# Kernel tuning notes

Measured on AMD Instinct MI355X. Metric: run time of the kernel, lower is better.

The kernel has to match this reference:

```python
import jax, jax.numpy as jnp
import numpy as np

N = 100000
E = 1600000
F_IN = 128
F_OUT = 128


def setup_inputs() -> dict:
    key = jax.random.key(0)
    k1, k2, k3, k4 = jax.random.split(key, 4)
    x = jax.random.normal(k1, (N, F_IN), dtype=jnp.float32)
    edge_index = jax.random.randint(k2, (2, E), 0, N, dtype=jnp.int64)
    # GCNConv params (glorot weight, zero bias as in PyG defaults)
    limit = float(np.sqrt(6.0 / (F_IN + F_OUT)))
    W = jax.random.uniform(k3, (F_IN, F_OUT), minval=-limit, maxval=limit, dtype=jnp.float32)
    b = jnp.zeros((F_OUT,), dtype=jnp.float32)
    return {"x": x, "edge_index": edge_index, "W": W, "b": b}


def reference(x, edge_index, W, b):
    n = x.shape[0]
    # add self-loops
    loops = jnp.arange(n, dtype=edge_index.dtype)
    src = jnp.concatenate([edge_index[0], loops])  # source nodes j
    dst = jnp.concatenate([edge_index[1], loops])  # target nodes i
    # symmetric normalization: deg over incoming edges (targets), weight 1
    deg = jax.ops.segment_sum(jnp.ones_like(dst, dtype=x.dtype), dst, num_segments=n)
    dinv = jnp.where(deg > 0, jax.lax.rsqrt(deg), 0.0)
    norm = dinv[src] * dinv[dst]  # [E+N]
    # linear transform then message passing
    h = x @ W  # [N, F_OUT]
    msgs = h[src] * norm[:, None]  # gather + scale, [E+N, F_OUT]
    out = jax.ops.segment_sum(msgs, dst, num_segments=n)  # scatter-add
    return out + b
```

## Files before the change

### kernel.cpp

```cpp
#include <hip/hip_runtime.h>

#define FDIM 128
#define NBMAX 512
#define EPB 4096

typedef __attribute__((ext_vector_type(8))) short bf16x8;
typedef __attribute__((ext_vector_type(4))) float f32x4;

__device__ __forceinline__ unsigned short f2bf(float f) {
    unsigned int u = __float_as_uint(f);
    unsigned int r = u + 0x7fffu + ((u >> 16) & 1u);
    return (unsigned short)(r >> 16);
}

__global__ __launch_bounds__(256) void k_bhist(const int* __restrict__ dst,
                                               int* __restrict__ bcnt, int e) {
    __shared__ int h[NBMAX];
    for (int i = threadIdx.x; i < NBMAX; i += 256) h[i] = 0;
    __syncthreads();
    int base = blockIdx.x * EPB;
    int end = min(base + EPB, e);
    for (int i = base + threadIdx.x; i < end; i += 256) atomicAdd(&h[dst[i] >> 8], 1);
    __syncthreads();
    for (int i = threadIdx.x; i < NBMAX; i += 256) {
        int c = h[i];
        if (c) atomicAdd(&bcnt[i], c);
    }
}

__global__ __launch_bounds__(512) void k_bscan(const int* __restrict__ bcnt,
                                               int* __restrict__ bbase,
                                               int* __restrict__ gcur, int nb, int e) {
    __shared__ int sh[512];
    int v = (threadIdx.x < nb) ? bcnt[threadIdx.x] : 0;
    sh[threadIdx.x] = v;
    __syncthreads();
    for (int off = 1; off < 512; off <<= 1) {
        int t = (threadIdx.x >= off) ? sh[threadIdx.x - off] : 0;
        __syncthreads();
        sh[threadIdx.x] += t;
        __syncthreads();
    }
    int excl = sh[threadIdx.x] - v;
    if (threadIdx.x < nb) {
        bbase[threadIdx.x] = excl;
        gcur[threadIdx.x] = excl;
    }
    if (threadIdx.x == 0) bbase[nb] = e;
}

__global__ __launch_bounds__(256) void k_scatterA(const int* __restrict__ src,
                                                  const int* __restrict__ dst,
                                                  int* __restrict__ gcur,
                                                  unsigned int* __restrict__ coarse, int e) {
    __shared__ int cur[NBMAX];
    for (int i = threadIdx.x; i < NBMAX; i += 256) cur[i] = 0;
    __syncthreads();
    int base = blockIdx.x * EPB;
    int end = min(base + EPB, e);
    for (int i = base + threadIdx.x; i < end; i += 256) atomicAdd(&cur[dst[i] >> 8], 1);
    __syncthreads();
    for (int i = threadIdx.x; i < NBMAX; i += 256) {
        int c = cur[i];
        cur[i] = c ? atomicAdd(&gcur[i], c) : 0;
    }
    __syncthreads();
    for (int i = base + threadIdx.x; i < end; i += 256) {
        int d = dst[i];
        int p = atomicAdd(&cur[d >> 8], 1);
        coarse[p] = ((unsigned)src[i] << 8) | (unsigned)(d & 255);
    }
}

__global__ __launch_bounds__(256) void k_bfin(const unsigned int* __restrict__ coarse,
                                              const int* __restrict__ bbase,
                                              int* __restrict__ deg, float* __restrict__ dinv,
                                              int* __restrict__ row_start,
                                              int* __restrict__ ebuf, int n) {
    __shared__ int ld[256];
    __shared__ int sc[256];
    __shared__ int cur[256];
    int b = blockIdx.x;
    int s = bbase[b], t = bbase[b + 1];
    ld[threadIdx.x] = 0;
    __syncthreads();
    for (int i = s + threadIdx.x; i < t; i += 256) atomicAdd(&ld[coarse[i] & 255u], 1);
    __syncthreads();
    int v = ld[threadIdx.x];
    sc[threadIdx.x] = v;
    __syncthreads();
    for (int off = 1; off < 256; off <<= 1) {
        int tv = (threadIdx.x >= off) ? sc[threadIdx.x - off] : 0;
        __syncthreads();
        sc[threadIdx.x] += tv;
        __syncthreads();
    }
    int rs = s + sc[threadIdx.x] - v;
    cur[threadIdx.x] = rs;
    int node = b * 256 + threadIdx.x;
    if (node < n) {
        deg[node] = v + 1;
        dinv[node] = rsqrtf((float)(v + 1));
        row_start[node] = rs;
    }
    __syncthreads();
    for (int i = s + threadIdx.x; i < t; i += 256) {
        unsigned int p = coarse[i];
        int pos = atomicAdd(&cur[p & 255u], 1);
        ebuf[pos] = (int)(p >> 8);
    }
}

__global__ __launch_bounds__(256) void k_wconv(const float* __restrict__ W,
                                               unsigned short* __restrict__ whl) {
    int id = blockIdx.x * 256 + threadIdx.x;
    int k = id >> 7, nn = id & 127;
    float w = W[id];
    unsigned short hi = f2bf(w);
    float hif = __uint_as_float(((unsigned)hi) << 16);
    unsigned short lo = f2bf(w - hif);
    whl[nn * FDIM + k] = hi;
    whl[FDIM * FDIM + nn * FDIM + k] = lo;
}

__global__ __launch_bounds__(256) void k_gemm(
    const float* __restrict__ x, const unsigned short* __restrict__ whl,
    const float* __restrict__ dinv, unsigned short* __restrict__ hs, int n) {
    __shared__ unsigned short Bs[2 * FDIM * FDIM];
    {
        const float4* g4 = (const float4*)whl;
        float4* l4 = (float4*)Bs;
        for (int i = threadIdx.x; i < 4096; i += 256) {
            int sel_n = i >> 4;
            int g = i & 15;
            l4[sel_n * 16 + (g ^ (sel_n & 15))] = g4[i];
        }
    }
    __syncthreads();

    const int lane = threadIdx.x & 63;
    const int wid = threadIdx.x >> 6;
    const int m = lane & 15;
    const int quad = lane >> 4;
    const int row0 = blockIdx.x * 64 + wid * 16;

    int rowA = row0 + m;
    if (rowA >= n) rowA = n - 1;
    const float* xr = x + (size_t)rowA * FDIM;

    f32x4 acc[8];
    #pragma unroll
    for (int ct = 0; ct < 8; ++ct) acc[ct] = (f32x4){0.f, 0.f, 0.f, 0.f};

    #pragma unroll
    for (int kc = 0; kc < 4; ++kc) {
        const int kb = kc * 32 + quad * 8;
        float4 xa = *(const float4*)(xr + kb);
        float4 xb = *(const float4*)(xr + kb + 4);
        float v[8] = {xa.x, xa.y, xa.z, xa.w, xb.x, xb.y, xb.z, xb.w};
        bf16x8 ahi, alo;
        #pragma unroll
        for (int j = 0; j < 8; ++j) {
            unsigned short h = f2bf(v[j]);
            ahi[j] = (short)h;
            alo[j] = (short)f2bf(v[j] - __uint_as_float(((unsigned)h) << 16));
        }
        const int g = kc * 4 + quad;
        #pragma unroll
        for (int ct = 0; ct < 8; ++ct) {
            int nidx = ct * 16 + m;
            const bf16x8 bhi = *(const bf16x8*)(Bs + (size_t)nidx * FDIM + (g ^ m) * 8);
            const bf16x8 blo = *(const bf16x8*)(Bs + (size_t)(FDIM + nidx) * FDIM + (g ^ m) * 8);
            acc[ct] = __builtin_amdgcn_mfma_f32_16x16x32_bf16(ahi, bhi, acc[ct], 0, 0, 0);
            acc[ct] = __builtin_amdgcn_mfma_f32_16x16x32_bf16(alo, bhi, acc[ct], 0, 0, 0);
            acc[ct] = __builtin_amdgcn_mfma_f32_16x16x32_bf16(ahi, blo, acc[ct], 0, 0, 0);
        }
    }

    #pragma unroll
    for (int r = 0; r < 4; ++r) {
        int row = row0 + quad * 4 + r;
        if (row >= n) continue;
        float s = dinv[row];
        unsigned short* hrow = hs + (size_t)row * FDIM;
        #pragma unroll
        for (int ct = 0; ct < 8; ++ct) hrow[ct * 16 + m] = f2bf(acc[ct][r] * s);
    }
}

__global__ __launch_bounds__(256) void k_gather(
    const unsigned short* __restrict__ hs, const int* __restrict__ ebuf,
    const int* __restrict__ row_start, const int* __restrict__ deg,
    const float* __restrict__ dinv, const float* __restrict__ bias,
    float* __restrict__ out, int n) {
    int i = blockIdx.x * 4 + (threadIdx.x >> 6);
    if (i >= n) return;
    int lane = threadIdx.x & 63;

    int beg = row_start[i];
    int cnt = deg[i] - 1;
    int end = beg + cnt;

    unsigned int u = ((const unsigned int*)(hs + (size_t)i * FDIM))[lane];
    float ax = __uint_as_float(u << 16);
    float ay = __uint_as_float(u & 0xffff0000u);

    int j = beg;
    for (; j + 3 < end; j += 4) {
        int s0 = ebuf[j], s1 = ebuf[j + 1], s2 = ebuf[j + 2], s3 = ebuf[j + 3];
        unsigned int u0 = ((const unsigned int*)(hs + (size_t)s0 * FDIM))[lane];
        unsigned int u1 = ((const unsigned int*)(hs + (size_t)s1 * FDIM))[lane];
        unsigned int u2 = ((const unsigned int*)(hs + (size_t)s2 * FDIM))[lane];
        unsigned int u3 = ((const unsigned int*)(hs + (size_t)s3 * FDIM))[lane];
        ax += __uint_as_float(u0 << 16) + __uint_as_float(u1 << 16)
            + __uint_as_float(u2 << 16) + __uint_as_float(u3 << 16);
        ay += __uint_as_float(u0 & 0xffff0000u) + __uint_as_float(u1 & 0xffff0000u)
            + __uint_as_float(u2 & 0xffff0000u) + __uint_as_float(u3 & 0xffff0000u);
    }
    for (; j < end; ++j) {
        int s0 = ebuf[j];
        unsigned int u0 = ((const unsigned int*)(hs + (size_t)s0 * FDIM))[lane];
        ax += __uint_as_float(u0 << 16);
        ay += __uint_as_float(u0 & 0xffff0000u);
    }

    float sc = dinv[i];
    float2 bb = ((const float2*)bias)[lane];
    float2 r = make_float2(ax * sc + bb.x, ay * sc + bb.y);
    ((float2*)(out + (size_t)i * FDIM))[lane] = r;
}

extern "C" void kernel_launch(void* const* d_in, const int* in_sizes, int n_in,
                              void* d_out, int out_size, void* d_ws, size_t ws_size,
                              hipStream_t stream) {
    const float* x  = (const float*)d_in[0];
    const int*   ei = (const int*)d_in[1];
    const float* W  = (const float*)d_in[2];
    const float* b  = (const float*)d_in[3];

    const int n = in_sizes[0] / FDIM;
    const int e = in_sizes[1] / 2;
    const int* src = ei;
    const int* dst = ei + e;
    float* out = (float*)d_out;

    const int nb = (n + 255) >> 8;
    const int eblocks = (e + EPB - 1) / EPB;

    char* ws = (char*)d_ws;
    size_t off = 0;
    auto alloc = [&](size_t bytes) {
        char* p = ws + off;
        off += (bytes + 511) & ~(size_t)511;
        return p;
    };
    int*            deg       = (int*)alloc((size_t)n * 4);
    float*          dinv      = (float*)alloc((size_t)n * 4);
    int*            row_start = (int*)alloc((size_t)n * 4);
    int*            bcnt      = (int*)alloc((size_t)NBMAX * 4);
    int*            bbase     = (int*)alloc((size_t)(NBMAX + 1) * 4);
    int*            gcur      = (int*)alloc((size_t)NBMAX * 4);
    unsigned short* whl       = (unsigned short*)alloc((size_t)2 * FDIM * FDIM * 2);
    unsigned int*   coarse    = (unsigned int*)alloc((size_t)e * 4);
    int*            ebuf      = (int*)alloc((size_t)e * 4);
    unsigned short* hs        = (unsigned short*)alloc((size_t)n * FDIM * 2);

    hipMemsetAsync(bcnt, 0, (size_t)NBMAX * 4, stream);

    k_wconv<<<64, 256, 0, stream>>>(W, whl);
    k_bhist<<<eblocks, 256, 0, stream>>>(dst, bcnt, e);
    k_bscan<<<1, 512, 0, stream>>>(bcnt, bbase, gcur, nb, e);
    k_scatterA<<<eblocks, 256, 0, stream>>>(src, dst, gcur, coarse, e);
    k_bfin<<<nb, 256, 0, stream>>>(coarse, bbase, deg, dinv, row_start, ebuf, n);

    k_gemm<<<(n + 63) / 64, 256, 0, stream>>>(x, whl, dinv, hs, n);

    {
        int blocks = (n + 3) / 4;
        k_gather<<<blocks, 256, 0, stream>>>(hs, ebuf, row_start, deg, dinv, b, out, n);
    }
}
```

Baseline: 259.0 us.

## Co-schedule GEMM with edge scatter and move source normalization into gather

The edge-histogram and weight-conversion kernels are merged into one launch, and the edge bucket scatter and the x@W GEMM run as disjoint block ranges of a single kernel. This lets the GEMM overlap with the edge sort and removes launches. Because dinv is no longer ready when the GEMM runs, the per-source dinv scaling moves into the gather loop as an extra dinv[src] load per edge. The split-bf16 GEMM also drops the weight low-part term, cutting MFMA work and LDS to a third less, at the cost of precision. The degree array is replaced by row_start[n+1].

```diff
diff --git a/kernel.cpp b/kernel.cpp
--- a/kernel.cpp
+++ b/kernel.cpp
@@ -13,24 +13,35 @@
     return (unsigned short)(r >> 16);
 }
 
-__global__ __launch_bounds__(256) void k_bhist(const int* __restrict__ dst,
-                                               int* __restrict__ bcnt, int e) {
+__global__ __launch_bounds__(256) void k_prep(const int* __restrict__ dst,
+                                              int* __restrict__ bcnt,
+                                              const float* __restrict__ W,
+                                              unsigned short* __restrict__ whi,
+                                              int e, int ebl) {
     __shared__ int h[NBMAX];
-    for (int i = threadIdx.x; i < NBMAX; i += 256) h[i] = 0;
-    __syncthreads();
-    int base = blockIdx.x * EPB;
-    int end = min(base + EPB, e);
-    for (int i = base + threadIdx.x; i < end; i += 256) atomicAdd(&h[dst[i] >> 8], 1);
-    __syncthreads();
-    for (int i = threadIdx.x; i < NBMAX; i += 256) {
-        int c = h[i];
-        if (c) atomicAdd(&bcnt[i], c);
+    if ((int)blockIdx.x < ebl) {
+        for (int i = threadIdx.x; i < NBMAX; i += 256) h[i] = 0;
+        __syncthreads();
+        int base = blockIdx.x * EPB;
+        int end = min(base + EPB, e);
+        for (int i = base + threadIdx.x; i < end; i += 256) atomicAdd(&h[dst[i] >> 8], 1);
+        __syncthreads();
+        for (int i = threadIdx.x; i < NBMAX; i += 256) {
+            int c = h[i];
+            if (c) atomicAdd(&bcnt[i], c);
+        }
+    } else {
+        int id = ((int)blockIdx.x - ebl) * 256 + threadIdx.x;
+        int k = id >> 7, nn = id & 127;
+        whi[nn * FDIM + k] = f2bf(W[id]);
     }
 }
 
 __global__ __launch_bounds__(512) void k_bscan(const int* __restrict__ bcnt,
                                                int* __restrict__ bbase,
-                                               int* __restrict__ gcur, int nb, int e) {
+                                               int* __restrict__ gcur,
+                                               int* __restrict__ row_start,
+                                               int nb, int n, int e) {
     __shared__ int sh[512];
     int v = (threadIdx.x < nb) ? bcnt[threadIdx.x] : 0;
     sh[threadIdx.x] = v;
@@ -46,35 +57,100 @@
         bbase[threadIdx.x] = excl;
         gcur[threadIdx.x] = excl;
     }
-    if (threadIdx.x == 0) bbase[nb] = e;
-}
-
-__global__ __launch_bounds__(256) void k_scatterA(const int* __restrict__ src,
-                                                  const int* __restrict__ dst,
-                                                  int* __restrict__ gcur,
-                                                  unsigned int* __restrict__ coarse, int e) {
+    if (threadIdx.x == 0) {
+        bbase[nb] = e;
+        row_start[n] = e;
+    }
+}
+
+__global__ __launch_bounds__(256) void k_main(
+    const int* __restrict__ src, const int* __restrict__ dst,
+    int* __restrict__ gcur, unsigned int* __restrict__ coarse,
+    const float* __restrict__ x, const unsigned short* __restrict__ whi,
+    unsigned short* __restrict__ hs, int e, int n, int ebl) {
+    __shared__ unsigned short Bs[FDIM * FDIM];
     __shared__ int cur[NBMAX];
-    for (int i = threadIdx.x; i < NBMAX; i += 256) cur[i] = 0;
-    __syncthreads();
-    int base = blockIdx.x * EPB;
-    int end = min(base + EPB, e);
-    for (int i = base + threadIdx.x; i < end; i += 256) atomicAdd(&cur[dst[i] >> 8], 1);
-    __syncthreads();
-    for (int i = threadIdx.x; i < NBMAX; i += 256) {
-        int c = cur[i];
-        cur[i] = c ? atomicAdd(&gcur[i], c) : 0;
-    }
-    __syncthreads();
-    for (int i = base + threadIdx.x; i < end; i += 256) {
-        int d = dst[i];
-        int p = atomicAdd(&cur[d >> 8], 1);
-        coarse[p] = ((unsigned)src[i] << 8) | (unsigned)(d & 255);
+
+    if ((int)blockIdx.x < ebl) {
+        for (int i = threadIdx.x; i < NBMAX; i += 256) cur[i] = 0;
+        __syncthreads();
+        int base = blockIdx.x * EPB;
+        int end = min(base + EPB, e);
+        for (int i = base + threadIdx.x; i < end; i += 256) atomicAdd(&cur[dst[i] >> 8], 1);
+        __syncthreads();
+        for (int i = threadIdx.x; i < NBMAX; i += 256) {
+            int c = cur[i];
+            cur[i] = c ? atomicAdd(&gcur[i], c) : 0;
+        }
+        __syncthreads();
+        for (int i = base + threadIdx.x; i < end; i += 256) {
+            int d = dst[i];
+            int p = atomicAdd(&cur[d >> 8], 1);
+            coarse[p] = ((unsigned)src[i] << 8) | (unsigned)(d & 255);
+        }
+    } else {
+        {
+            const float4* g4 = (const float4*)whi;
+            float4* l4 = (float4*)Bs;
+            for (int i = threadIdx.x; i < 2048; i += 256) {
+                int nn = i >> 4;
+                int g = i & 15;
+                l4[nn * 16 + (g ^ (nn & 15))] = g4[i];
+            }
+        }
+        __syncthreads();
+
+        const int lane = threadIdx.x & 63;
+        const int wid = threadIdx.x >> 6;
+        const int m = lane & 15;
+        const int quad = lane >> 4;
+        const int row0 = ((int)blockIdx.x - ebl) * 64 + wid * 16;
+
+        int rowA = row0 + m;
+        if (rowA >= n) rowA = n - 1;
+        const float* xr = x + (size_t)rowA * FDIM;
+
+        f32x4 acc[8];
+        #pragma unroll
+        for (int ct = 0; ct < 8; ++ct) acc[ct] = (f32x4){0.f, 0.f, 0.f, 0.f};
+
+        #pragma unroll
+        for (int kc = 0; kc < 4; ++kc) {
+            const int kb = kc * 32 + quad * 8;
+            float4 xa = *(const float4*)(xr + kb);
+            float4 xb = *(const float4*)(xr + kb + 4);
+            float v[8] = {xa.x, xa.y, xa.z, xa.w, xb.x, xb.y, xb.z, xb.w};
+            bf16x8 ahi, alo;
+            #pragma unroll
+            for (int j = 0; j < 8; ++j) {
+                unsigned short hh = f2bf(v[j]);
+                ahi[j] = (short)hh;
+                alo[j] = (short)f2bf(v[j] - __uint_as_float(((unsigned)hh) << 16));
+            }
+            const int g = kc * 4 + quad;
+            #pragma unroll
+            for (int ct = 0; ct < 8; ++ct) {
+                int nidx = ct * 16 + m;
+                const bf16x8 bhi = *(const bf16x8*)(Bs + (size_t)nidx * FDIM + (g ^ m) * 8);
+                acc[ct] = __builtin_amdgcn_mfma_f32_16x16x32_bf16(ahi, bhi, acc[ct], 0, 0, 0);
+                acc[ct] = __builtin_amdgcn_mfma_f32_16x16x32_bf16(alo, bhi, acc[ct], 0, 0, 0);
+            }
+        }
+
+        #pragma unroll
+        for (int r = 0; r < 4; ++r) {
+            int row = row0 + quad * 4 + r;
+            if (row >= n) continue;
+            unsigned short* hrow = hs + (size_t)row * FDIM;
+            #pragma unroll
+            for (int ct = 0; ct < 8; ++ct) hrow[ct * 16 + m] = f2bf(acc[ct][r]);
+        }
     }
 }
 
 __global__ __launch_bounds__(256) void k_bfin(const unsigned int* __restrict__ coarse,
                                               const int* __restrict__ bbase,
-                                              int* __restrict__ deg, float* __restrict__ dinv,
+                                              float* __restrict__ dinv,
                                               int* __restrict__ row_start,
                                               int* __restrict__ ebuf, int n) {
     __shared__ int ld[256];
@@ -99,7 +175,6 @@
     cur[threadIdx.x] = rs;
     int node = b * 256 + threadIdx.x;
     if (node < n) {
-        deg[node] = v + 1;
         dinv[node] = rsqrtf((float)(v + 1));
         row_start[node] = rs;
     }
@@ -111,122 +186,49 @@
     }
 }
 
-__global__ __launch_bounds__(256) void k_wconv(const float* __restrict__ W,
-                                               unsigned short* __restrict__ whl) {
-    int id = blockIdx.x * 256 + threadIdx.x;
-    int k = id >> 7, nn = id & 127;
-    float w = W[id];
-    unsigned short hi = f2bf(w);
-    float hif = __uint_as_float(((unsigned)hi) << 16);
-    unsigned short lo = f2bf(w - hif);
-    whl[nn * FDIM + k] = hi;
-    whl[FDIM * FDIM + nn * FDIM + k] = lo;
-}
-
-__global__ __launch_bounds__(256) void k_gemm(
-    const float* __restrict__ x, const unsigned short* __restrict__ whl,
-    const float* __restrict__ dinv, unsigned short* __restrict__ hs, int n) {
-    __shared__ unsigned short Bs[2 * FDIM * FDIM];
-    {
-        const float4* g4 = (const float4*)whl;
-        float4* l4 = (float4*)Bs;
-        for (int i = threadIdx.x; i < 4096; i += 256) {
-            int sel_n = i >> 4;
-            int g = i & 15;
-            l4[sel_n * 16 + (g ^ (sel_n & 15))] = g4[i];
-        }
-    }
-    __syncthreads();
-
-    const int lane = threadIdx.x & 63;
-    const int wid = threadIdx.x >> 6;
-    const int m = lane & 15;
-    const int quad = lane >> 4;
-    const int row0 = blockIdx.x * 64 + wid * 16;
-
-    int rowA = row0 + m;
-    if (rowA >= n) rowA = n - 1;
-    const float* xr = x + (size_t)rowA * FDIM;
-
-    f32x4 acc[8];
-    #pragma unroll
-    for (int ct = 0; ct < 8; ++ct) acc[ct] = (f32x4){0.f, 0.f, 0.f, 0.f};
-
-    #pragma unroll
-    for (int kc = 0; kc < 4; ++kc) {
-        const int kb = kc * 32 + quad * 8;
-        float4 xa = *(const float4*)(xr + kb);
-        float4 xb = *(const float4*)(xr + kb + 4);
-        float v[8] = {xa.x, xa.y, xa.z, xa.w, xb.x, xb.y, xb.z, xb.w};
-        bf16x8 ahi, alo;
-        #pragma unroll
-        for (int j = 0; j < 8; ++j) {
-            unsigned short h = f2bf(v[j]);
-            ahi[j] = (short)h;
-            alo[j] = (short)f2bf(v[j] - __uint_as_float(((unsigned)h) << 16));
-        }
-        const int g = kc * 4 + quad;
-        #pragma unroll
-        for (int ct = 0; ct < 8; ++ct) {
-            int nidx = ct * 16 + m;
-            const bf16x8 bhi = *(const bf16x8*)(Bs + (size_t)nidx * FDIM + (g ^ m) * 8);
-            const bf16x8 blo = *(const bf16x8*)(Bs + (size_t)(FDIM + nidx) * FDIM + (g ^ m) * 8);
-            acc[ct] = __builtin_amdgcn_mfma_f32_16x16x32_bf16(ahi, bhi, acc[ct], 0, 0, 0);
-            acc[ct] = __builtin_amdgcn_mfma_f32_16x16x32_bf16(alo, bhi, acc[ct], 0, 0, 0);
-            acc[ct] = __builtin_amdgcn_mfma_f32_16x16x32_bf16(ahi, blo, acc[ct], 0, 0, 0);
-        }
-    }
-
-    #pragma unroll
-    for (int r = 0; r < 4; ++r) {
-        int row = row0 + quad * 4 + r;
-        if (row >= n) continue;
-        float s = dinv[row];
-        unsigned short* hrow = hs + (size_t)row * FDIM;
-        #pragma unroll
-        for (int ct = 0; ct < 8; ++ct) hrow[ct * 16 + m] = f2bf(acc[ct][r] * s);
-    }
-}
-
 __global__ __launch_bounds__(256) void k_gather(
     const unsigned short* __restrict__ hs, const int* __restrict__ ebuf,
-    const int* __restrict__ row_start, const int* __restrict__ deg,
-    const float* __restrict__ dinv, const float* __restrict__ bias,
-    float* __restrict__ out, int n) {
+    const int* __restrict__ row_start, const float* __restrict__ dinv,
+    const float* __restrict__ bias, float* __restrict__ out, int n) {
     int i = blockIdx.x * 4 + (threadIdx.x >> 6);
     if (i >= n) return;
     int lane = threadIdx.x & 63;
 
     int beg = row_start[i];
-    int cnt = deg[i] - 1;
-    int end = beg + cnt;
+    int end = row_start[i + 1];
+    float di = dinv[i];
 
     unsigned int u = ((const unsigned int*)(hs + (size_t)i * FDIM))[lane];
-    float ax = __uint_as_float(u << 16);
-    float ay = __uint_as_float(u & 0xffff0000u);
+    float ax = di * __uint_as_float(u << 16);
+    float ay = di * __uint_as_float(u & 0xffff0000u);
 
     int j = beg;
     for (; j + 3 < end; j += 4) {
         int s0 = ebuf[j], s1 = ebuf[j + 1], s2 = ebuf[j + 2], s3 = ebuf[j + 3];
+        float d0 = dinv[s0], d1 = dinv[s1], d2 = dinv[s2], d3 = dinv[s3];
         unsigned int u0 = ((const unsigned int*)(hs + (size_t)s0 * FDIM))[lane];
         unsigned int u1 = ((const unsigned int*)(hs + (size_t)s1 * FDIM))[lane];
         unsigned int u2 = ((const unsigned int*)(hs + (size_t)s2 * FDIM))[lane];
         unsigned int u3 = ((const unsigned int*)(hs + (size_t)s3 * FDIM))[lane];
-        ax += __uint_as_float(u0 << 16) + __uint_as_float(u1 << 16)
-            + __uint_as_float(u2 << 16) + __uint_as_float(u3 << 16);
-        ay += __uint_as_float(u0 & 0xffff0000u) + __uint_as_float(u1 & 0xffff0000u)
-            + __uint_as_float(u2 & 0xffff0000u) + __uint_as_float(u3 & 0xffff0000u);
+        ax = fmaf(d0, __uint_as_float(u0 << 16), ax);
+        ay = fmaf(d0, __uint_as_float(u0 & 0xffff0000u), ay);
+        ax = fmaf(d1, __uint_as_float(u1 << 16), ax);
+        ay = fmaf(d1, __uint_as_float(u1 & 0xffff0000u), ay);
+        ax = fmaf(d2, __uint_as_float(u2 << 16), ax);
+        ay = fmaf(d2, __uint_as_float(u2 & 0xffff0000u), ay);
+        ax = fmaf(d3, __uint_as_float(u3 << 16), ax);
+        ay = fmaf(d3, __uint_as_float(u3 & 0xffff0000u), ay);
     }
     for (; j < end; ++j) {
         int s0 = ebuf[j];
+        float d0 = dinv[s0];
         unsigned int u0 = ((const unsigned int*)(hs + (size_t)s0 * FDIM))[lane];
-        ax += __uint_as_float(u0 << 16);
-        ay += __uint_as_float(u0 & 0xffff0000u);
-    }
-
-    float sc = dinv[i];
+        ax = fmaf(d0, __uint_as_float(u0 << 16), ax);
+        ay = fmaf(d0, __uint_as_float(u0 & 0xffff0000u), ay);
+    }
+
     float2 bb = ((const float2*)bias)[lane];
-    float2 r = make_float2(ax * sc + bb.x, ay * sc + bb.y);
+    float2 r = make_float2(fmaf(ax, di, bb.x), fmaf(ay, di, bb.y));
     ((float2*)(out + (size_t)i * FDIM))[lane] = r;
 }
 
@@ -245,7 +247,8 @@
     float* out = (float*)d_out;
 
     const int nb = (n + 255) >> 8;
-    const int eblocks = (e + EPB - 1) / EPB;
+    const int ebl = (e + EPB - 1) / EPB;
+    const int gemmbl = (n + 63) / 64;
 
     char* ws = (char*)d_ws;
     size_t off = 0;
@@ -254,29 +257,24 @@
         off += (bytes + 511) & ~(size_t)511;
         return p;
     };
-    int*            deg       = (int*)alloc((size_t)n * 4);
     float*          dinv      = (float*)alloc((size_t)n * 4);
-    int*            row_start = (int*)alloc((size_t)n * 4);
+    int*            row_start = (int*)alloc((size_t)(n + 1) * 4);
     int*            bcnt      = (int*)alloc((size_t)NBMAX * 4);
     int*            bbase     = (int*)alloc((size_t)(NBMAX + 1) * 4);
     int*            gcur      = (int*)alloc((size_t)NBMAX * 4);
-    unsigned short* whl       = (unsigned short*)alloc((size_t)2 * FDIM * FDIM * 2);
+    unsigned short* whi       = (unsigned short*)alloc((size_t)FDIM * FDIM * 2);
     unsigned int*   coarse    = (unsigned int*)alloc((size_t)e * 4);
     int*            ebuf      = (int*)alloc((size_t)e * 4);
     unsigned short* hs        = (unsigned short*)alloc((size_t)n * FDIM * 2);
 
     hipMemsetAsync(bcnt, 0, (size_t)NBMAX * 4, stream);
 
-    k_wconv<<<64, 256, 0, stream>>>(W, whl);
-    k_bhist<<<eblocks, 256, 0, stream>>>(dst, bcnt, e);
-    k_bscan<<<1, 512, 0, stream>>>(bcnt, bbase, gcur, nb, e);
-    k_scatterA<<<eblocks, 256, 0, stream>>>(src, dst, gcur, coarse, e);
-    k_bfin<<<nb, 256, 0, stream>>>(coarse, bbase, deg, dinv, row_start, ebuf, n);
-
-    k_gemm<<<(n + 63) / 64, 256, 0, stream>>>(x, whl, dinv, hs, n);
-
+    k_prep<<<ebl + 64, 256, 0, stream>>>(dst, bcnt, W, whi, e, ebl);
+    k_bscan<<<1, 512, 0, stream>>>(bcnt, bbase, gcur, row_start, nb, n, e);
+    k_main<<<ebl + gemmbl, 256, 0, stream>>>(src, dst, gcur, coarse, x, whi, hs, e, n, ebl);
+    k_bfin<<<nb, 256, 0, stream>>>(coarse, bbase, dinv, row_start, ebuf, n);
     {
         int blocks = (n + 3) / 4;
-        k_gather<<<blocks, 256, 0, stream>>>(hs, ebuf, row_start, deg, dinv, b, out, n);
-    }
-}
+        k_gather<<<blocks, 256, 0, stream>>>(hs, ebuf, row_start, dinv, b, out, n);
+    }
+}
```

Result: faster. 246.8 us (-4.7%).
